# Kernel optimization log

Measured on AMD Instinct MI355X. Metric: run time of the kernel, lower is better.

The kernel has to match this reference:

```python
import jax, jax.numpy as jnp
import numpy as np

D_MODEL = 1024
N_HEADS = 16
D_FF = 4096
HEAD_DIM = D_MODEL // N_HEADS
EPS = 1e-5


def setup_inputs() -> dict:
    key = jax.random.key(0)
    ks = jax.random.split(key, 12)
    B, S, D = 2, 2048, D_MODEL
    s = 0.02
    return {
        "x": jax.random.normal(ks[0], (B, S, D), jnp.float32),
        "ln1_g": jnp.ones((D,), jnp.float32),
        "ln1_b": jnp.zeros((D,), jnp.float32),
        "qkv_w": jax.random.normal(ks[1], (3 * D, D), jnp.float32) * s,
        "qkv_b": jnp.zeros((3 * D,), jnp.float32),
        "out_w": jax.random.normal(ks[2], (D, D), jnp.float32) * s,
        "out_b": jnp.zeros((D,), jnp.float32),
        "ln2_g": jnp.ones((D,), jnp.float32),
        "ln2_b": jnp.zeros((D,), jnp.float32),
        "fc1_w": jax.random.normal(ks[3], (D_FF, D), jnp.float32) * s,
        "fc1_b": jnp.zeros((D_FF,), jnp.float32),
        "fc2_w": jax.random.normal(ks[4], (D, D_FF), jnp.float32) * s,
        "fc2_b": jnp.zeros((D,), jnp.float32),
    }


def _layernorm(x, g, b):
    mu = jnp.mean(x, axis=-1, keepdims=True)
    var = jnp.mean(jnp.square(x - mu), axis=-1, keepdims=True)
    return (x - mu) * jax.lax.rsqrt(var + EPS) * g + b


def _attention(h, qkv_w, qkv_b, out_w, out_b):
    B, S, D = h.shape
    qkv = h @ qkv_w.T + qkv_b  # [B,S,3D]
    q, k, v = jnp.split(qkv, 3, axis=-1)
    # [B,H,S,hd]
    q = q.reshape(B, S, N_HEADS, HEAD_DIM).transpose(0, 2, 1, 3)
    k = k.reshape(B, S, N_HEADS, HEAD_DIM).transpose(0, 2, 1, 3)
    v = v.reshape(B, S, N_HEADS, HEAD_DIM).transpose(0, 2, 1, 3)
    scale = HEAD_DIM ** -0.5
    scores = jnp.einsum("bhqd,bhkd->bhqk", q, k) * scale
    causal = jnp.tril(jnp.ones((S, S), bool))
    scores = jnp.where(causal, scores, -jnp.inf)
    attn = jax.nn.softmax(scores, axis=-1)
    out = jnp.einsum("bhqk,bhkd->bhqd", attn, v)
    out = out.transpose(0, 2, 1, 3).reshape(B, S, D)
    return out @ out_w.T + out_b


def reference(x, ln1_g, ln1_b, qkv_w, qkv_b, out_w, out_b,
              ln2_g, ln2_b, fc1_w, fc1_b, fc2_w, fc2_b):
    x = x + _attention(_layernorm(x, ln1_g, ln1_b), qkv_w, qkv_b, out_w, out_b)
    h = _layernorm(x, ln2_g, ln2_b)
    ff = jax.nn.gelu(h @ fc1_w.T + fc1_b, approximate=False) @ fc2_w.T + fc2_b
    return x + ff
```

## Files before the change

### kernel.cpp

```cpp
#include <hip/hip_runtime.h>
#include <stdint.h>

typedef uint16_t u16;
typedef uint32_t u32;
typedef __bf16 bf16_t;
typedef bf16_t bf16x8 __attribute__((ext_vector_type(8)));
typedef float f32x4 __attribute__((ext_vector_type(4)));
typedef u16 u16x4 __attribute__((ext_vector_type(4)));
typedef u16 u16x8 __attribute__((ext_vector_type(8)));

__device__ __forceinline__ float bf2f(u16 v) {
    union { u32 u; float f; } x; x.u = ((u32)v) << 16; return x.f;
}
__device__ __forceinline__ u16 f2bf(float f) {
    union { float f; u32 u; } x; x.f = f;
    u32 r = (x.u + 0x7fffu + ((x.u >> 16) & 1u)) >> 16;
    return (u16)r;
}

__device__ __forceinline__ void gload_lds16(const u16* g, u16* l) {
    __builtin_amdgcn_global_load_lds(
        (const __attribute__((address_space(1))) void*)g,
        (__attribute__((address_space(3))) void*)l,
        16, 0, 0);
}
#define WAIT_ALL() __builtin_amdgcn_s_waitcnt(0)

__global__ __launch_bounds__(256) void cvt_kernel(
    const float* __restrict__ src, u16* __restrict__ dst, int n4)
{
    int i = blockIdx.x * 256 + threadIdx.x;
    if (i >= n4) return;
    f32x4 v = ((const f32x4*)src)[i];
    u16x4 o;
#pragma unroll
    for (int j = 0; j < 4; j++) o[j] = f2bf(v[j]);
    ((u16x4*)dst)[i] = o;
}

__global__ __launch_bounds__(256) void ln_kernel(
    const float* __restrict__ x, const float* __restrict__ g,
    const float* __restrict__ b, u16* __restrict__ out)
{
    const int row = blockIdx.x;
    const int tid = threadIdx.x;
    f32x4 xv = *(const f32x4*)(x + (size_t)row * 1024 + tid * 4);
    float v[4];
    float s = 0.f, s2 = 0.f;
#pragma unroll
    for (int i = 0; i < 4; i++) { v[i] = xv[i]; s += v[i]; s2 += v[i] * v[i]; }
#pragma unroll
    for (int off = 1; off < 64; off <<= 1) {
        s  += __shfl_xor(s, off);
        s2 += __shfl_xor(s2, off);
    }
    __shared__ float ws1[4], ws2[4];
    if ((tid & 63) == 0) { ws1[tid >> 6] = s; ws2[tid >> 6] = s2; }
    __syncthreads();
    s  = ws1[0] + ws1[1] + ws1[2] + ws1[3];
    s2 = ws2[0] + ws2[1] + ws2[2] + ws2[3];
    float mu  = s * (1.0f / 1024.0f);
    float var = s2 * (1.0f / 1024.0f) - mu * mu;
    float rstd = rsqrtf(var + 1e-5f);
    f32x4 gv = *(const f32x4*)(g + tid * 4);
    f32x4 bv = *(const f32x4*)(b + tid * 4);
    u16x4 ov;
#pragma unroll
    for (int i = 0; i < 4; i++)
        ov[i] = f2bf((v[i] - mu) * rstd * gv[i] + bv[i]);
    *(u16x4*)(out + (size_t)row * 1024 + tid * 4) = ov;
}

__global__ __launch_bounds__(256, 2) void gemm_bt(
    const u16* __restrict__ A, const u16* __restrict__ Bt,
    const float* __restrict__ bias, const float* res,
    void* C, int N, int K, int lda, int gelu)
{
    __shared__ __align__(16) u16 sA[128 * 32];
    __shared__ __align__(16) u16 sB[128 * 32];
    const int tid  = threadIdx.x;
    const int wave = tid >> 6, lane = tid & 63;
    const int lm = lane & 15, quad = lane >> 4;
    const int wm = wave >> 1, wn = wave & 1;
    const int row0 = blockIdx.y * 128, col0 = blockIdx.x * 128;
    const int r16 = lane >> 2;
    const int c8  = (lane & 3) * 8;

    f32x4 acc[4][4];
#pragma unroll
    for (int i = 0; i < 4; i++)
#pragma unroll
        for (int j = 0; j < 4; j++) acc[i][j] = f32x4{0.f, 0.f, 0.f, 0.f};

    for (int k0 = 0; k0 < K; k0 += 32) {
        __syncthreads();
        if (wave < 2) {
#pragma unroll
            for (int j = 0; j < 4; j++) {
                int chunk = wave * 4 + j;
                int r = chunk * 16 + r16;
                gload_lds16(A + (size_t)(row0 + r) * lda + k0 + c8, &sA[chunk * 512]);
            }
        } else {
#pragma unroll
            for (int j = 0; j < 4; j++) {
                int chunk = (wave - 2) * 4 + j;
                int r = chunk * 16 + r16;
                gload_lds16(Bt + (size_t)(col0 + r) * K + k0 + c8, &sB[chunk * 512]);
            }
        }
        WAIT_ALL();
        __syncthreads();

        bf16x8 af[4], bfr[4];
#pragma unroll
        for (int t = 0; t < 4; t++)
            af[t] = *(const bf16x8*)&sA[(wm * 64 + t * 16 + lm) * 32 + quad * 8];
#pragma unroll
        for (int t = 0; t < 4; t++)
            bfr[t] = *(const bf16x8*)&sB[(wn * 64 + t * 16 + lm) * 32 + quad * 8];
#pragma unroll
        for (int i = 0; i < 4; i++)
#pragma unroll
            for (int j = 0; j < 4; j++)
                acc[i][j] = __builtin_amdgcn_mfma_f32_16x16x32_bf16(af[i], bfr[j], acc[i][j], 0, 0, 0);
    }

    float bj[4];
#pragma unroll
    for (int j = 0; j < 4; j++) bj[j] = bias[col0 + wn * 64 + j * 16 + lm];
#pragma unroll
    for (int i = 0; i < 4; i++) {
        int rbase = row0 + wm * 64 + i * 16 + quad * 4;
#pragma unroll
        for (int j = 0; j < 4; j++) {
            int c = col0 + wn * 64 + j * 16 + lm;
#pragma unroll
            for (int r = 0; r < 4; r++) {
                float v = acc[i][j][r] + bj[j];
                if (gelu) v = 0.5f * v * (1.0f + erff(v * 0.70710678118f));
                size_t idx = (size_t)(rbase + r) * N + c;
                if (res) {
                    ((float*)C)[idx] = v + res[idx];
                } else {
                    ((u16*)C)[idx] = f2bf(v);
                }
            }
        }
    }
}

__global__ __launch_bounds__(256, 2) void gemm_bt64(
    const u16* __restrict__ A, const u16* __restrict__ Bt,
    const float* __restrict__ bias, const float* res,
    void* C, int N, int K, int lda, int gelu)
{
    __shared__ __align__(16) u16 sA[128 * 32];
    __shared__ __align__(16) u16 sB[64 * 32];
    const int tid  = threadIdx.x;
    const int wave = tid >> 6, lane = tid & 63;
    const int lm = lane & 15, quad = lane >> 4;
    const int wm = wave >> 1, wn = wave & 1;
    const int row0 = blockIdx.y * 128, col0 = blockIdx.x * 64;
    const int r16 = lane >> 2;
    const int c8  = (lane & 3) * 8;

    f32x4 acc[4][2];
#pragma unroll
    for (int i = 0; i < 4; i++)
#pragma unroll
        for (int j = 0; j < 2; j++) acc[i][j] = f32x4{0.f, 0.f, 0.f, 0.f};

    for (int k0 = 0; k0 < K; k0 += 32) {
        __syncthreads();
#pragma unroll
        for (int j = 0; j < 3; j++) {
            int cid = wave * 3 + j;
            if (cid < 8) {
                int r = cid * 16 + r16;
                gload_lds16(A + (size_t)(row0 + r) * lda + k0 + c8, &sA[cid * 512]);
            } else {
                int bc = cid - 8;
                int r = bc * 16 + r16;
                gload_lds16(Bt + (size_t)(col0 + r) * K + k0 + c8, &sB[bc * 512]);
            }
        }
        WAIT_ALL();
        __syncthreads();

        bf16x8 af[4], bfr[2];
#pragma unroll
        for (int t = 0; t < 4; t++)
            af[t] = *(const bf16x8*)&sA[(wm * 64 + t * 16 + lm) * 32 + quad * 8];
#pragma unroll
        for (int t = 0; t < 2; t++)
            bfr[t] = *(const bf16x8*)&sB[(wn * 32 + t * 16 + lm) * 32 + quad * 8];
#pragma unroll
        for (int i = 0; i < 4; i++)
#pragma unroll
            for (int j = 0; j < 2; j++)
                acc[i][j] = __builtin_amdgcn_mfma_f32_16x16x32_bf16(af[i], bfr[j], acc[i][j], 0, 0, 0);
    }

    float bj[2];
#pragma unroll
    for (int j = 0; j < 2; j++) bj[j] = bias[col0 + wn * 32 + j * 16 + lm];
#pragma unroll
    for (int i = 0; i < 4; i++) {
        int rbase = row0 + wm * 64 + i * 16 + quad * 4;
#pragma unroll
        for (int j = 0; j < 2; j++) {
            int c = col0 + wn * 32 + j * 16 + lm;
#pragma unroll
            for (int r = 0; r < 4; r++) {
                float v = acc[i][j][r] + bj[j];
                if (gelu) v = 0.5f * v * (1.0f + erff(v * 0.70710678118f));
                size_t idx = (size_t)(rbase + r) * N + c;
                if (res) {
                    ((float*)C)[idx] = v + res[idx];
                } else {
                    ((u16*)C)[idx] = f2bf(v);
                }
            }
        }
    }
}

__global__ __launch_bounds__(256, 4) void attn_kernel(u16* qkv)
{
    __shared__ __align__(16) u16 sQ[64 * 64];
    __shared__ __align__(16) u16 sK[64 * 64];
    __shared__ __align__(16) u16 sVT[64 * 64];
    __shared__ __align__(16) u16 sP[4 * 16 * 72];

    const int tid  = threadIdx.x;
    const int wave = tid >> 6, lane = tid & 63;
    const int lm = lane & 15, quad = lane >> 4;
    int xi = blockIdx.x;
    int qz = (xi & 1) ? (31 - (xi >> 1)) : (xi >> 1);
    int qi = ((blockIdx.y >> 3) & 1) ? (31 - qz) : qz;
    const int q0 = qi * 64;
    const int b = blockIdx.y >> 4, h = blockIdx.y & 15;
    const size_t tok0 = (size_t)b * 2048;
    const int qcol = h * 64, kcol = 1024 + h * 64, vcol = 2048 + h * 64;
    const int r8 = lane >> 3;
    const int c8 = (lane & 7) * 8;

#pragma unroll
    for (int j = 0; j < 2; j++) {
        int chunk = wave * 2 + j;
        int r = chunk * 8 + r8;
        gload_lds16(qkv + (tok0 + q0 + r) * 3072 + qcol + c8, &sQ[chunk * 512]);
    }
    WAIT_ALL();
    __syncthreads();

    bf16x8 aq[2];
#pragma unroll
    for (int kk = 0; kk < 2; kk++)
        aq[kk] = *(const bf16x8*)&sQ[(wave * 16 + lm) * 64 + kk * 32 + quad * 8];

    f32x4 oacc[4];
    float mrun[4], lrun[4];
#pragma unroll
    for (int n = 0; n < 4; n++) oacc[n] = f32x4{0.f, 0.f, 0.f, 0.f};
#pragma unroll
    for (int r = 0; r < 4; r++) { mrun[r] = -1e30f; lrun[r] = 0.f; }

    const int vkey = tid >> 2;
    const int vdq  = (tid & 3) * 16;
    const int vpos = (((vkey >> 3) ^ (tid & 3)) << 3) | (vkey & 7);

    u16* sPw = &sP[wave * 16 * 72];
    const int ntiles = qi + 1;

    for (int tk = 0; tk < ntiles; tk++) {
        const int kb = tk * 64;
        __syncthreads();
#pragma unroll
        for (int j = 0; j < 2; j++) {
            int chunk = wave * 2 + j;
            int r = chunk * 8 + r8;
            gload_lds16(qkv + (tok0 + kb + r) * 3072 + kcol + c8, &sK[chunk * 512]);
        }
        {
            const u16* vr = qkv + (tok0 + kb + vkey) * 3072 + vcol + vdq;
            u16x8 v0 = *(const u16x8*)vr;
            u16x8 v1 = *(const u16x8*)(vr + 8);
#pragma unroll
            for (int i = 0; i < 8; i++) sVT[(vdq + i) * 64 + vpos] = v0[i];
#pragma unroll
            for (int i = 0; i < 8; i++) sVT[(vdq + 8 + i) * 64 + vpos] = v1[i];
        }
        WAIT_ALL();
        __syncthreads();

        float sc[4][4];
#pragma unroll
        for (int n = 0; n < 4; n++) {
            f32x4 s = f32x4{0.f, 0.f, 0.f, 0.f};
#pragma unroll
            for (int kk = 0; kk < 2; kk++) {
                bf16x8 bk = *(const bf16x8*)&sK[(n * 16 + lm) * 64 + kk * 32 + quad * 8];
                s = __builtin_amdgcn_mfma_f32_16x16x32_bf16(aq[kk], bk, s, 0, 0, 0);
            }
            int col  = kb + n * 16 + lm;
            int rowb = q0 + wave * 16 + quad * 4;
#pragma unroll
            for (int r = 0; r < 4; r++)
                sc[n][r] = (col <= rowb + r) ? s[r] * 0.125f : -1e30f;
        }
#pragma unroll
        for (int r = 0; r < 4; r++) {
            float mx = fmaxf(fmaxf(sc[0][r], sc[1][r]), fmaxf(sc[2][r], sc[3][r]));
#pragma unroll
            for (int off = 1; off < 16; off <<= 1) mx = fmaxf(mx, __shfl_xor(mx, off));
            float mnew  = fmaxf(mrun[r], mx);
            float alpha = __expf(mrun[r] - mnew);
            float sum = 0.f;
#pragma unroll
            for (int n = 0; n < 4; n++) {
                float p = __expf(sc[n][r] - mnew);
                sc[n][r] = p;
                sum += p;
            }
#pragma unroll
            for (int off = 1; off < 16; off <<= 1) sum += __shfl_xor(sum, off);
            lrun[r] = lrun[r] * alpha + sum;
            mrun[r] = mnew;
#pragma unroll
            for (int n = 0; n < 4; n++) oacc[n][r] *= alpha;
        }
#pragma unroll
        for (int n = 0; n < 4; n++)
#pragma unroll
            for (int r = 0; r < 4; r++)
                sPw[(quad * 4 + r) * 72 + n * 16 + lm] = f2bf(sc[n][r]);
        bf16x8 ap[2];
#pragma unroll
        for (int kk = 0; kk < 2; kk++)
            ap[kk] = *(const bf16x8*)&sPw[lm * 72 + kk * 32 + quad * 8];
#pragma unroll
        for (int n = 0; n < 4; n++)
#pragma unroll
            for (int kk = 0; kk < 2; kk++) {
                bf16x8 bv = *(const bf16x8*)
                    &sVT[(n * 16 + lm) * 64 + (((kk * 4 + quad) ^ n) << 3)];
                oacc[n] = __builtin_amdgcn_mfma_f32_16x16x32_bf16(ap[kk], bv, oacc[n], 0, 0, 0);
            }
    }

    {
        int rowb = q0 + wave * 16 + quad * 4;
#pragma unroll
        for (int r = 0; r < 4; r++) {
            float inv = 1.0f / lrun[r];
#pragma unroll
            for (int n = 0; n < 4; n++) {
                int d = n * 16 + lm;
                qkv[(tok0 + rowb + r) * 3072 + qcol + d] = f2bf(oacc[n][r] * inv);
            }
        }
    }
}

extern "C" void kernel_launch(void* const* d_in, const int* in_sizes, int n_in,
                              void* d_out, int out_size, void* d_ws, size_t ws_size,
                              hipStream_t stream)
{
    (void)in_sizes; (void)n_in; (void)out_size; (void)ws_size;
    const float* x    = (const float*)d_in[0];
    const float* ln1g = (const float*)d_in[1];
    const float* ln1b = (const float*)d_in[2];
    const float* qkvwF= (const float*)d_in[3];
    const float* qkvb = (const float*)d_in[4];
    const float* outwF= (const float*)d_in[5];
    const float* outb = (const float*)d_in[6];
    const float* ln2g = (const float*)d_in[7];
    const float* ln2b = (const float*)d_in[8];
    const float* fc1wF= (const float*)d_in[9];
    const float* fc1b = (const float*)d_in[10];
    const float* fc2wF= (const float*)d_in[11];
    const float* fc2b = (const float*)d_in[12];
    float* out = (float*)d_out;
    u16*   ws  = (u16*)d_ws;
    const int M1 = 1 << 20;

    u16* qkvw = ws;
    u16* outw = ws + 3 * M1;
    u16* qkvB = ws + 4 * M1;
    u16* ff1  = ws;
    u16* fc1w = ws + 16 * M1;
    u16* fc2w = ws + 20 * M1;
    u16* h    = ws + 24 * M1;

    cvt_kernel<<<3072, 256, 0, stream>>>(qkvwF, qkvw, 3 * M1 / 4);
    cvt_kernel<<<1024, 256, 0, stream>>>(outwF, outw, 1 * M1 / 4);
    cvt_kernel<<<4096, 256, 0, stream>>>(fc1wF, fc1w, 4 * M1 / 4);
    cvt_kernel<<<4096, 256, 0, stream>>>(fc2wF, fc2w, 4 * M1 / 4);

    ln_kernel<<<4096, 256, 0, stream>>>(x, ln1g, ln1b, h);
    gemm_bt<<<dim3(24, 32), 256, 0, stream>>>(h, qkvw, qkvb, nullptr, qkvB,
                                              3072, 1024, 1024, 0);
    attn_kernel<<<dim3(32, 32), 256, 0, stream>>>(qkvB);
    gemm_bt64<<<dim3(16, 32), 256, 0, stream>>>(qkvB, outw, outb, x, out,
                                                1024, 1024, 3072, 0);
    ln_kernel<<<4096, 256, 0, stream>>>(out, ln2g, ln2b, h);
    gemm_bt<<<dim3(32, 32), 256, 0, stream>>>(h, fc1w, fc1b, nullptr, ff1,
                                              4096, 1024, 1024, 1);
    gemm_bt64<<<dim3(16, 32), 256, 0, stream>>>(ff1, fc2w, fc2b, out, out,
                                                1024, 4096, 4096, 0);
}
```

Baseline: 439.3 us.

## Double-buffer LDS tiles in GEMM kernels to overlap global loads with MFMA

Both GEMM kernels now keep two LDS buffers for the A and B tiles and issue the direct-to-LDS global loads for the next K step before computing on the current one. A partial vmcnt wait lets the current tile's loads finish while the prefetch is still in flight. The intent is to hide global memory latency behind MFMA work instead of stalling on a full wait every iteration. The cost is double the shared memory per block, which may reduce occupancy, plus a second barrier per iteration. There is also some risk around ordering of the asynchronous LDS writes.

Result: faster. 401.8 us (-8.6%).

```diff
diff --git a/kernel.cpp b/kernel.cpp
--- a/kernel.cpp
+++ b/kernel.cpp
@@ -25,6 +25,8 @@
         16, 0, 0);
 }
 #define WAIT_ALL() __builtin_amdgcn_s_waitcnt(0)
+#define WAITVM(n) __builtin_amdgcn_s_waitcnt(0x0F70 | (n))
+#define BARRIER() __builtin_amdgcn_s_barrier()
 
 __global__ __launch_bounds__(256) void cvt_kernel(
     const float* __restrict__ src, u16* __restrict__ dst, int n4)
@@ -76,8 +78,8 @@
     const float* __restrict__ bias, const float* res,
     void* C, int N, int K, int lda, int gelu)
 {
-    __shared__ __align__(16) u16 sA[128 * 32];
-    __shared__ __align__(16) u16 sB[128 * 32];
+    __shared__ __align__(16) u16 sA[2][128 * 32];
+    __shared__ __align__(16) u16 sB[2][128 * 32];
     const int tid  = threadIdx.x;
     const int wave = tid >> 6, lane = tid & 63;
     const int lm = lane & 15, quad = lane >> 4;
@@ -85,6 +87,22 @@
     const int row0 = blockIdx.y * 128, col0 = blockIdx.x * 128;
     const int r16 = lane >> 2;
     const int c8  = (lane & 3) * 8;
+    const int niter = K >> 5;
+
+    const u16* gsrc;
+    size_t gstride;
+    int chunk0;
+    if (wave < 2) {
+        chunk0 = wave * 4;
+        gsrc = A + (size_t)(row0 + chunk0 * 16 + r16) * lda + c8;
+        gstride = lda;
+    } else {
+        chunk0 = (wave - 2) * 4;
+        gsrc = Bt + (size_t)(col0 + chunk0 * 16 + r16) * K + c8;
+        gstride = K;
+    }
+    u16* lbase0 = (wave < 2) ? &sA[0][chunk0 * 512] : &sB[0][chunk0 * 512];
+    u16* lbase1 = (wave < 2) ? &sA[1][chunk0 * 512] : &sB[1][chunk0 * 512];
 
     f32x4 acc[4][4];
 #pragma unroll
@@ -92,38 +110,38 @@
 #pragma unroll
         for (int j = 0; j < 4; j++) acc[i][j] = f32x4{0.f, 0.f, 0.f, 0.f};
 
-    for (int k0 = 0; k0 < K; k0 += 32) {
-        __syncthreads();
-        if (wave < 2) {
-#pragma unroll
-            for (int j = 0; j < 4; j++) {
-                int chunk = wave * 4 + j;
-                int r = chunk * 16 + r16;
-                gload_lds16(A + (size_t)(row0 + r) * lda + k0 + c8, &sA[chunk * 512]);
-            }
+#pragma unroll
+    for (int j = 0; j < 4; j++)
+        gload_lds16(gsrc + (size_t)(j * 16) * gstride, lbase0 + j * 512);
+
+    for (int k = 0; k < niter; k++) {
+        const int cur = k & 1;
+        if (k + 1 < niter) {
+            const u16* gs = gsrc + (size_t)(k + 1) * 32;
+            u16* lb = cur ? lbase0 : lbase1;
+#pragma unroll
+            for (int j = 0; j < 4; j++)
+                gload_lds16(gs + (size_t)(j * 16) * gstride, lb + j * 512);
+            WAITVM(4);
         } else {
-#pragma unroll
-            for (int j = 0; j < 4; j++) {
-                int chunk = (wave - 2) * 4 + j;
-                int r = chunk * 16 + r16;
-                gload_lds16(Bt + (size_t)(col0 + r) * K + k0 + c8, &sB[chunk * 512]);
-            }
-        }
-        WAIT_ALL();
-        __syncthreads();
+            WAITVM(0);
+        }
+        BARRIER();
 
         bf16x8 af[4], bfr[4];
 #pragma unroll
         for (int t = 0; t < 4; t++)
-            af[t] = *(const bf16x8*)&sA[(wm * 64 + t * 16 + lm) * 32 + quad * 8];
+            af[t] = *(const bf16x8*)&sA[cur][(wm * 64 + t * 16 + lm) * 32 + quad * 8];
 #pragma unroll
         for (int t = 0; t < 4; t++)
-            bfr[t] = *(const bf16x8*)&sB[(wn * 64 + t * 16 + lm) * 32 + quad * 8];
+            bfr[t] = *(const bf16x8*)&sB[cur][(wn * 64 + t * 16 + lm) * 32 + quad * 8];
 #pragma unroll
         for (int i = 0; i < 4; i++)
 #pragma unroll
             for (int j = 0; j < 4; j++)
                 acc[i][j] = __builtin_amdgcn_mfma_f32_16x16x32_bf16(af[i], bfr[j], acc[i][j], 0, 0, 0);
+
+        BARRIER();
     }
 
     float bj[4];
@@ -155,8 +173,8 @@
     const float* __restrict__ bias, const float* res,
     void* C, int N, int K, int lda, int gelu)
 {
-    __shared__ __align__(16) u16 sA[128 * 32];
-    __shared__ __align__(16) u16 sB[64 * 32];
+    __shared__ __align__(16) u16 sA[2][128 * 32];
+    __shared__ __align__(16) u16 sB[2][64 * 32];
     const int tid  = threadIdx.x;
     const int wave = tid >> 6, lane = tid & 63;
     const int lm = lane & 15, quad = lane >> 4;
@@ -164,6 +182,28 @@
     const int row0 = blockIdx.y * 128, col0 = blockIdx.x * 64;
     const int r16 = lane >> 2;
     const int c8  = (lane & 3) * 8;
+    const int niter = K >> 5;
+
+    const u16* gs_[3];
+    u16* lb0_[3];
+    u16* lb1_[3];
+    size_t gstride_[3];
+#pragma unroll
+    for (int j = 0; j < 3; j++) {
+        int cid = wave * 3 + j;
+        if (cid < 8) {
+            gs_[j] = A + (size_t)(row0 + cid * 16 + r16) * lda + c8;
+            gstride_[j] = lda;
+            lb0_[j] = &sA[0][cid * 512];
+            lb1_[j] = &sA[1][cid * 512];
+        } else {
+            int bc = cid - 8;
+            gs_[j] = Bt + (size_t)(col0 + bc * 16 + r16) * K + c8;
+            gstride_[j] = K;
+            lb0_[j] = &sB[0][bc * 512];
+            lb1_[j] = &sB[1][bc * 512];
+        }
+    }
 
     f32x4 acc[4][2];
 #pragma unroll
@@ -171,35 +211,35 @@
 #pragma unroll
         for (int j = 0; j < 2; j++) acc[i][j] = f32x4{0.f, 0.f, 0.f, 0.f};
 
-    for (int k0 = 0; k0 < K; k0 += 32) {
-        __syncthreads();
-#pragma unroll
-        for (int j = 0; j < 3; j++) {
-            int cid = wave * 3 + j;
-            if (cid < 8) {
-                int r = cid * 16 + r16;
-                gload_lds16(A + (size_t)(row0 + r) * lda + k0 + c8, &sA[cid * 512]);
-            } else {
-                int bc = cid - 8;
-                int r = bc * 16 + r16;
-                gload_lds16(Bt + (size_t)(col0 + r) * K + k0 + c8, &sB[bc * 512]);
-            }
-        }
-        WAIT_ALL();
-        __syncthreads();
+#pragma unroll
+    for (int j = 0; j < 3; j++) gload_lds16(gs_[j], lb0_[j]);
+
+    for (int k = 0; k < niter; k++) {
+        const int cur = k & 1;
+        if (k + 1 < niter) {
+#pragma unroll
+            for (int j = 0; j < 3; j++)
+                gload_lds16(gs_[j] + (size_t)(k + 1) * 32, cur ? lb0_[j] : lb1_[j]);
+            WAITVM(3);
+        } else {
+            WAITVM(0);
+        }
+        BARRIER();
 
         bf16x8 af[4], bfr[2];
 #pragma unroll
         for (int t = 0; t < 4; t++)
-            af[t] = *(const bf16x8*)&sA[(wm * 64 + t * 16 + lm) * 32 + quad * 8];
+            af[t] = *(const bf16x8*)&sA[cur][(wm * 64 + t * 16 + lm) * 32 + quad * 8];
 #pragma unroll
         for (int t = 0; t < 2; t++)
-            bfr[t] = *(const bf16x8*)&sB[(wn * 32 + t * 16 + lm) * 32 + quad * 8];
+            bfr[t] = *(const bf16x8*)&sB[cur][(wn * 32 + t * 16 + lm) * 32 + quad * 8];
 #pragma unroll
         for (int i = 0; i < 4; i++)
 #pragma unroll
             for (int j = 0; j < 2; j++)
                 acc[i][j] = __builtin_amdgcn_mfma_f32_16x16x32_bf16(af[i], bfr[j], acc[i][j], 0, 0, 0);
+
+        BARRIER();
     }
 
     float bj[2];
```
